# Kernel optimization log

Measured on AMD Instinct MI355X. Metric: run time of the kernel, lower is better.

Reference implementation:

```python
import jax, jax.numpy as jnp
import numpy as np

B, ZD, E, L, NL = 64, 512, 512, 8192, 1000


def irm(x, Ws, bs):
    # IRMLinear(d, n_layers=2): stack of residual linear blocks x <- x + Linear(x)
    for W, b in zip(Ws, bs):
        x = x + x @ W.T + b
    return x


def setup_inputs() -> dict:
    key = jax.random.key(0)
    ks = jax.random.split(key, 10)
    s = lambda k, sh: (jax.random.normal(k, sh, jnp.float32) * 0.02)
    return dict(
        z=jax.random.normal(ks[0], (B, ZD), jnp.float32),
        y=jax.random.randint(ks[1], (B,), 0, NL),
        W_yemb=s(ks[2], (E, NL)), b_yemb=jnp.zeros((E,), jnp.float32),
        Wy1=s(ks[3], (E, E)), by1=jnp.zeros((E,), jnp.float32),
        Wy2=s(ks[4], (E, E)), by2=jnp.zeros((E,), jnp.float32),
        Wz1=s(ks[5], (ZD, ZD)), bz1=jnp.zeros((ZD,), jnp.float32),
        Wz2=s(ks[6], (ZD, ZD)), bz2=jnp.zeros((ZD,), jnp.float32),
        W_zlat=s(ks[7], (L, ZD)),          # Linear(z_dim, lat_size, bias=False)
        w_proj=s(ks[8], (E,)),             # Linear(embed_size, 1, bias=False)
    )


def reference(z, y, W_yemb, b_yemb, Wy1, by1, Wy2, by2, Wz1, bz1, Wz2, bz2, W_zlat, w_proj):
    # y: int64 class ids -> one-hot via identity embedding_mat
    yembed = jax.nn.one_hot(y, NL, dtype=jnp.float32)            # [B, NL]
    ye = yembed @ W_yemb.T + b_yemb                               # [B, E]
    ye = irm(ye, [Wy1, Wy2], [by1, by2])                          # [B, E]
    zz = irm(z, [Wz1, Wz2], [bz1, bz2])                           # [B, ZD]
    zl = zz @ W_zlat.T                                            # [B, L]
    # bmm(z[:,:,1], ye[:,1,:]) then lat_proj over embed collapses to a
    # per-batch scalar: lat[b,i] = zl[b,i] * (ye[b] . w_proj)  (same math,
    # avoids the [B, L, E] intermediate)
    s_scal = ye @ w_proj                                          # [B]
    return zl * s_scal[:, None]                                   # [B, L]
```

## Files before the change

### kernel.cpp

```cpp
#include <hip/hip_runtime.h>


#define BB 64
#define DD 512
#define LL 8192
#define NLBL 1000
#define PIT 68

typedef __attribute__((ext_vector_type(8))) short short8;
typedef __attribute__((ext_vector_type(4))) float f32x4;

__device__ __forceinline__ unsigned short f2bf(float f) {
  unsigned u = __float_as_uint(f);
  return (unsigned short)((u + 0x7fffu + ((u >> 16) & 1u)) >> 16);
}

__device__ __forceinline__ void matvec_block(int eblk, const float* __restrict__ W,
                                             const float* __restrict__ vin,
                                             float* __restrict__ vout) {
  __shared__ float vl[DD];
  __shared__ float red[256];
  int tid = threadIdx.x;
  vl[tid] = vin[tid];
  vl[tid + 256] = vin[tid + 256];
  __syncthreads();
  int el = tid & 31, jg = tid >> 5;
  int e = eblk * 32 + el;
  float acc = 0.f;
  for (int j = jg; j < DD; j += 8)
    acc += W[j * DD + e] * vl[j];
  red[tid] = acc;
  __syncthreads();
  if (tid < 32) {
    float s = vl[eblk * 32 + tid];
#pragma unroll
    for (int g = 0; g < 8; ++g) s += red[g * 32 + tid];
    vout[eblk * 32 + tid] = s;
  }
}

template <int FIRST>
__device__ __forceinline__ void layer_gemm(int blk, const float* __restrict__ Xg,
                                           const float* __restrict__ P1,
                                           const float* __restrict__ W,
                                           const float* __restrict__ bias,
                                           float* __restrict__ P) {
  __shared__ __align__(16) float Xs[BB][PIT];
  __shared__ __align__(16) float Ws[32][PIT];
  int tid = threadIdx.x;
  int jt = blk >> 3, ks = blk & 7;
  int j0 = jt * 32, k0 = ks * 64;
#pragma unroll
  for (int i = 0; i < 4; ++i) {
    int slot = tid + i * 256, row = slot >> 4, c4 = (slot & 15) * 4;
    float4 v;
    if (FIRST) {
      v = *(const float4*)&Xg[row * DD + k0 + c4];
    } else {
      v = float4{0.f, 0.f, 0.f, 0.f};
#pragma unroll
      for (int s = 0; s < 8; ++s) {
        float4 p = *(const float4*)&P1[(s * BB + row) * DD + k0 + c4];
        v.x += p.x; v.y += p.y; v.z += p.z; v.w += p.w;
      }
    }
    *(float4*)&Xs[row][c4] = v;
  }
#pragma unroll
  for (int i = 0; i < 2; ++i) {
    int slot = tid + i * 256, row = slot >> 4, c4 = (slot & 15) * 4;
    *(float4*)&Ws[row][c4] = *(const float4*)&W[(j0 + row) * DD + k0 + c4];
  }
  __syncthreads();
  int jl = tid & 15, bl = tid >> 4;
  float acc[4][2] = {};
#pragma unroll
  for (int k = 0; k < 64; k += 4) {
    float4 xv[4], wv[2];
#pragma unroll
    for (int i = 0; i < 4; ++i) xv[i] = *(const float4*)&Xs[bl + 16 * i][k];
#pragma unroll
    for (int u = 0; u < 2; ++u) wv[u] = *(const float4*)&Ws[jl + 16 * u][k];
#pragma unroll
    for (int i = 0; i < 4; ++i)
#pragma unroll
      for (int u = 0; u < 2; ++u)
        acc[i][u] += xv[i].x * wv[u].x + xv[i].y * wv[u].y +
                     xv[i].z * wv[u].z + xv[i].w * wv[u].w;
  }
#pragma unroll
  for (int i = 0; i < 4; ++i) {
    int b = bl + 16 * i;
#pragma unroll
    for (int u = 0; u < 2; ++u) {
      int jj = j0 + jl + 16 * u;
      float v = acc[i][u];
      if (ks == 0) {
        float xr;
        if (FIRST) {
          xr = Xg[b * DD + jj];
        } else {
          xr = 0.f;
#pragma unroll
          for (int s = 0; s < 8; ++s) xr += P1[(s * BB + b) * DD + jj];
        }
        v += xr + bias[jj];
      }
      P[(ks * BB + b) * DD + jj] = v;
    }
  }
}

__global__ __launch_bounds__(256) void kA(const float* __restrict__ z,
                                          const float* __restrict__ Wz1,
                                          const float* __restrict__ bz1,
                                          float* __restrict__ P1,
                                          const float* __restrict__ Wy2,
                                          const float* __restrict__ w_proj,
                                          float* __restrict__ u1) {
  int blk = blockIdx.x;
  if (blk < 128) layer_gemm<1>(blk, z, nullptr, Wz1, bz1, P1);
  else           matvec_block(blk - 128, Wy2, w_proj, u1);
}

__global__ __launch_bounds__(256) void kB(const float* __restrict__ P1,
                                          const float* __restrict__ Wz2,
                                          const float* __restrict__ bz2,
                                          float* __restrict__ P2,
                                          const float* __restrict__ Wy1,
                                          const float* __restrict__ u1,
                                          float* __restrict__ u0,
                                          const float* __restrict__ by1,
                                          const float* __restrict__ by2,
                                          const float* __restrict__ w_proj,
                                          float* __restrict__ d2) {
  int blk = blockIdx.x;
  if (blk < 128) {
    layer_gemm<0>(blk, nullptr, P1, Wz2, bz2, P2);
  } else if (blk < 144) {
    matvec_block(blk - 128, Wy1, u1, u0);
  } else {
    __shared__ float red[256];
    int tid = threadIdx.x;
    float p = by1[tid] * u1[tid] + by2[tid] * w_proj[tid] +
              by1[tid + 256] * u1[tid + 256] + by2[tid + 256] * w_proj[tid + 256];
    red[tid] = p;
    __syncthreads();
    if (tid < 64) {
      float s = red[tid] + red[tid + 64] + red[tid + 128] + red[tid + 192];
#pragma unroll
      for (int d = 32; d; d >>= 1) s += __shfl_down(s, d, 64);
      if (tid == 0) d2[0] = s;
    }
  }
}

__global__ __launch_bounds__(256) void kZ(const float* __restrict__ P2,
                                          unsigned short* __restrict__ zzbf,
                                          const float* __restrict__ W_yemb,
                                          const float* __restrict__ b_yemb,
                                          const int* __restrict__ y,
                                          const float* __restrict__ u0,
                                          const float* __restrict__ d2,
                                          float* __restrict__ sbv) {
  int blk = blockIdx.x, tid = threadIdx.x;
  if (blk < 16) {
    int e0 = blk * 2048 + tid * 8;
    float4 a0 = {0.f, 0.f, 0.f, 0.f}, a1 = {0.f, 0.f, 0.f, 0.f};
#pragma unroll
    for (int s = 0; s < 8; ++s) {
      const float* p = P2 + s * (BB * DD) + e0;
      float4 x = *(const float4*)p;
      float4 yv = *(const float4*)(p + 4);
      a0.x += x.x; a0.y += x.y; a0.z += x.z; a0.w += x.w;
      a1.x += yv.x; a1.y += yv.y; a1.z += yv.z; a1.w += yv.w;
    }
    short8 h = {(short)f2bf(a0.x), (short)f2bf(a0.y), (short)f2bf(a0.z),
                (short)f2bf(a0.w), (short)f2bf(a1.x), (short)f2bf(a1.y),
                (short)f2bf(a1.z), (short)f2bf(a1.w)};
    *(short8*)&zzbf[e0] = h;
    return;
  }
  __shared__ float u0l[DD];
  u0l[tid] = u0[tid];
  u0l[tid + 256] = u0[tid + 256];
  __syncthreads();
  int bl = tid >> 5, el = tid & 31;
  int b = (blk - 16) * 8 + bl;
  int yb = y[b];
  float acc = 0.f;
  for (int e = el; e < DD; e += 32)
    acc += (W_yemb[(size_t)e * NLBL + yb] + b_yemb[e]) * u0l[e];
#pragma unroll
  for (int d = 16; d; d >>= 1) acc += __shfl_down(acc, d, 32);
  if (el == 0) sbv[b] = acc + d2[0];
}

__global__ __launch_bounds__(256) void kC(const unsigned short* __restrict__ zzbf,
                                          const float* __restrict__ W,
                                          const float* __restrict__ sbv,
                                          float* __restrict__ out) {
  __shared__ __align__(16) unsigned short As[64 * 128];
  __shared__ __align__(16) unsigned short Bs[32 * 128];
  int tid = threadIdx.x;
  int l0 = blockIdx.x * 32;
  int wave = tid >> 6, lane = tid & 63;
  int quad = lane >> 4, l15 = lane & 15;
  f32x4 acc[2] = {};
  for (int kc = 0; kc < 4; ++kc) {
    int k0 = kc * 128;
#pragma unroll
    for (int i = 0; i < 2; ++i) {
      int slot = tid + i * 256, row = slot >> 4, g = slot & 15;
      const float* src = &W[(size_t)(l0 + row) * DD + k0 + g * 8];
      float4 v0 = *(const float4*)src;
      float4 v1 = *(const float4*)(src + 4);
      short8 h = {(short)f2bf(v0.x), (short)f2bf(v0.y), (short)f2bf(v0.z),
                  (short)f2bf(v0.w), (short)f2bf(v1.x), (short)f2bf(v1.y),
                  (short)f2bf(v1.z), (short)f2bf(v1.w)};
      *(short8*)&Bs[row * 128 + ((g ^ (row & 15)) << 3)] = h;
    }
#pragma unroll
    for (int i = 0; i < 4; ++i) {
      int slot = tid + i * 256, row = slot >> 4, g = slot & 15;
      short8 h = *(const short8*)&zzbf[row * DD + k0 + g * 8];
      *(short8*)&As[row * 128 + ((g ^ (row & 15)) << 3)] = h;
    }
    __syncthreads();
#pragma unroll
    for (int s = 0; s < 4; ++s) {
      int g = s * 4 + quad;
      short8 af = *(const short8*)&As[(wave * 16 + l15) * 128 +
                                      ((g ^ l15) << 3)];
#pragma unroll
      for (int ni = 0; ni < 2; ++ni) {
        short8 bf = *(const short8*)&Bs[(ni * 16 + l15) * 128 +
                                        ((g ^ l15) << 3)];
        acc[ni] = __builtin_amdgcn_mfma_f32_16x16x32_bf16(af, bf, acc[ni], 0, 0, 0);
      }
    }
    __syncthreads();
  }
#pragma unroll
  for (int ni = 0; ni < 2; ++ni) {
#pragma unroll
    for (int reg = 0; reg < 4; ++reg) {
      int b = wave * 16 + quad * 4 + reg;
      out[(size_t)b * LL + l0 + ni * 16 + l15] = sbv[b] * acc[ni][reg];
    }
  }
}

extern "C" void kernel_launch(void* const* d_in, const int* in_sizes, int n_in,
                              void* d_out, int out_size, void* d_ws, size_t ws_size,
                              hipStream_t stream) {
  const float* z      = (const float*)d_in[0];
  const int*   y      = (const int*)  d_in[1];
  const float* W_yemb = (const float*)d_in[2];
  const float* b_yemb = (const float*)d_in[3];
  const float* Wy1    = (const float*)d_in[4];
  const float* by1    = (const float*)d_in[5];
  const float* Wy2    = (const float*)d_in[6];
  const float* by2    = (const float*)d_in[7];
  const float* Wz1    = (const float*)d_in[8];
  const float* bz1    = (const float*)d_in[9];
  const float* Wz2    = (const float*)d_in[10];
  const float* bz2    = (const float*)d_in[11];
  const float* W_zlat = (const float*)d_in[12];
  const float* w_proj = (const float*)d_in[13];

  float* ws = (float*)d_ws;
  float* P1 = ws;
  float* P2 = ws + 262144;
  unsigned short* zzbf = (unsigned short*)(ws + 524288);
  float* u1 = ws + 524288 + 16384;
  float* u0 = u1 + 512;
  float* sb = u0 + 512;
  float* d2 = sb + 64;
  float* out = (float*)d_out;

  kA<<<144, 256, 0, stream>>>(z, Wz1, bz1, P1, Wy2, w_proj, u1);
  kB<<<145, 256, 0, stream>>>(P1, Wz2, bz2, P2, Wy1, u1, u0, by1, by2, w_proj, d2);
  kZ<<<24, 256, 0, stream>>>(P2, zzbf, W_yemb, b_yemb, y, u0, d2, sb);
  kC<<<256, 256, 0, stream>>>(zzbf, W_zlat, sb, out);
}
```

Measured before the change: 143.6 us.

## Fuse four launches into one persistent kernel with atomic-counter grid barriers

Replaces the four kernel launches with a single kernel. 256 blocks preload and convert their W_zlat tile to bf16 in shared memory while 145 chain blocks run the two IRM layers, the y-side matvecs and the scalar reduction, separated by global atomic-counter barriers. The per-batch scale is folded into the bf16 zz rows before the final MFMA GEMM, and A fragments are read straight from global memory instead of being staged in LDS. This removes launch gaps and overlaps the large W_zlat load with the serial chain, but it relies on all 401 blocks being co-resident (deadlock risk otherwise), adds spin-waiting and a memset, and applying the scale before bf16 rounding changes rounding slightly.

```diff
diff --git a/kernel.cpp b/kernel.cpp
--- a/kernel.cpp
+++ b/kernel.cpp
@@ -6,6 +6,8 @@
 #define LL 8192
 #define NLBL 1000
 #define PIT 68
+#define NKC 256
+#define NCHAIN 145
 
 typedef __attribute__((ext_vector_type(8))) short short8;
 typedef __attribute__((ext_vector_type(4))) float f32x4;
@@ -15,11 +17,27 @@
   return (unsigned short)((u + 0x7fffu + ((u >> 16) & 1u)) >> 16);
 }
 
-__device__ __forceinline__ void matvec_block(int eblk, const float* __restrict__ W,
+__device__ __forceinline__ unsigned ld_agent(const unsigned* p) {
+  return __hip_atomic_load(p, __ATOMIC_RELAXED, __HIP_MEMORY_SCOPE_AGENT);
+}
+
+__device__ __forceinline__ void chain_barrier(unsigned* c) {
+  __syncthreads();
+  if (threadIdx.x == 0) {
+    __threadfence();
+    atomicAdd(c, 1u);
+    while (ld_agent(c) < NCHAIN) __builtin_amdgcn_s_sleep(1);
+    __threadfence();
+  }
+  __syncthreads();
+}
+
+__device__ __forceinline__ void matvec_block(char* SM, int eblk,
+                                             const float* __restrict__ W,
                                              const float* __restrict__ vin,
                                              float* __restrict__ vout) {
-  __shared__ float vl[DD];
-  __shared__ float red[256];
+  float* vl = (float*)SM;
+  float* red = vl + DD;
   int tid = threadIdx.x;
   vl[tid] = vin[tid];
   vl[tid + 256] = vin[tid + 256];
@@ -40,13 +58,14 @@
 }
 
 template <int FIRST>
-__device__ __forceinline__ void layer_gemm(int blk, const float* __restrict__ Xg,
-                                           const float* __restrict__ P1,
+__device__ __forceinline__ void layer_gemm(char* SM, int blk,
+                                           const float* __restrict__ Xg,
+                                           const float* __restrict__ Pin,
                                            const float* __restrict__ W,
                                            const float* __restrict__ bias,
                                            float* __restrict__ P) {
-  __shared__ __align__(16) float Xs[BB][PIT];
-  __shared__ __align__(16) float Ws[32][PIT];
+  float (*Xs)[PIT] = (float (*)[PIT])SM;
+  float (*Ws)[PIT] = (float (*)[PIT])(SM + BB * PIT * 4);
   int tid = threadIdx.x;
   int jt = blk >> 3, ks = blk & 7;
   int j0 = jt * 32, k0 = ks * 64;
@@ -60,7 +79,7 @@
       v = float4{0.f, 0.f, 0.f, 0.f};
 #pragma unroll
       for (int s = 0; s < 8; ++s) {
-        float4 p = *(const float4*)&P1[(s * BB + row) * DD + k0 + c4];
+        float4 p = *(const float4*)&Pin[(s * BB + row) * DD + k0 + c4];
         v.x += p.x; v.y += p.y; v.z += p.z; v.w += p.w;
       }
     }
@@ -102,7 +121,7 @@
         } else {
           xr = 0.f;
 #pragma unroll
-          for (int s = 0; s < 8; ++s) xr += P1[(s * BB + b) * DD + jj];
+          for (int s = 0; s < 8; ++s) xr += Pin[(s * BB + b) * DD + jj];
         }
         v += xr + bias[jj];
       }
@@ -111,37 +130,85 @@
   }
 }
 
-__global__ __launch_bounds__(256) void kA(const float* __restrict__ z,
-                                          const float* __restrict__ Wz1,
-                                          const float* __restrict__ bz1,
-                                          float* __restrict__ P1,
-                                          const float* __restrict__ Wy2,
-                                          const float* __restrict__ w_proj,
-                                          float* __restrict__ u1) {
-  int blk = blockIdx.x;
-  if (blk < 128) layer_gemm<1>(blk, z, nullptr, Wz1, bz1, P1);
-  else           matvec_block(blk - 128, Wy2, w_proj, u1);
-}
-
-__global__ __launch_bounds__(256) void kB(const float* __restrict__ P1,
-                                          const float* __restrict__ Wz2,
-                                          const float* __restrict__ bz2,
-                                          float* __restrict__ P2,
-                                          const float* __restrict__ Wy1,
-                                          const float* __restrict__ u1,
-                                          float* __restrict__ u0,
-                                          const float* __restrict__ by1,
-                                          const float* __restrict__ by2,
-                                          const float* __restrict__ w_proj,
-                                          float* __restrict__ d2) {
-  int blk = blockIdx.x;
-  if (blk < 128) {
-    layer_gemm<0>(blk, nullptr, P1, Wz2, bz2, P2);
-  } else if (blk < 144) {
-    matvec_block(blk - 128, Wy1, u1, u0);
+__global__ __launch_bounds__(256, 2) void mega(
+    const float* __restrict__ z, const float* __restrict__ Wz1,
+    const float* __restrict__ bz1, const float* __restrict__ Wz2,
+    const float* __restrict__ bz2, const float* __restrict__ Wy1,
+    const float* __restrict__ by1, const float* __restrict__ Wy2,
+    const float* __restrict__ by2, const float* __restrict__ w_proj,
+    const float* __restrict__ W_yemb, const float* __restrict__ b_yemb,
+    const int* __restrict__ y, const float* __restrict__ W_zlat,
+    float* __restrict__ P1, float* __restrict__ P2,
+    unsigned short* __restrict__ zzs, float* __restrict__ u1,
+    float* __restrict__ u0, float* __restrict__ d2,
+    unsigned* __restrict__ cnt, float* __restrict__ out) {
+  __shared__ __align__(16) char SM[32768];
+  int blk = blockIdx.x, tid = threadIdx.x;
+
+  if (blk < NKC) {
+    unsigned short* Bs = (unsigned short*)SM;
+    int l0 = blk * 32;
+#pragma unroll
+    for (int i = 0; i < 8; ++i) {
+      int gi = tid + i * 256;
+      int row = gi >> 6, c = gi & 63;
+      const float* src = &W_zlat[(size_t)(l0 + row) * DD + c * 8];
+      float4 v0 = *(const float4*)src;
+      float4 v1 = *(const float4*)(src + 4);
+      short8 h = {(short)f2bf(v0.x), (short)f2bf(v0.y), (short)f2bf(v0.z),
+                  (short)f2bf(v0.w), (short)f2bf(v1.x), (short)f2bf(v1.y),
+                  (short)f2bf(v1.z), (short)f2bf(v1.w)};
+      *(short8*)&Bs[row * DD + ((c ^ (row & 7)) << 3)] = h;
+    }
+    if (tid == 0) {
+      while (ld_agent(&cnt[64]) < NCHAIN) __builtin_amdgcn_s_sleep(2);
+      __threadfence();
+    }
+    __syncthreads();
+    int wave = tid >> 6, lane = tid & 63, quad = lane >> 4, l15 = lane & 15;
+    const unsigned short* arow = zzs + (wave * 16 + l15) * DD + quad * 8;
+    int brow0 = l15, brow1 = 16 + l15;
+    f32x4 acc0 = {}, acc1 = {};
+    short8 apf[4];
+#pragma unroll
+    for (int p = 0; p < 4; ++p) apf[p] = *(const short8*)(arow + p * 32);
+#pragma unroll
+    for (int kc = 0; kc < 4; ++kc) {
+      short8 cur[4] = {apf[0], apf[1], apf[2], apf[3]};
+      if (kc < 3) {
+#pragma unroll
+        for (int p = 0; p < 4; ++p)
+          apf[p] = *(const short8*)(arow + (kc + 1) * 128 + p * 32);
+      }
+#pragma unroll
+      for (int s = 0; s < 4; ++s) {
+        int c = kc * 16 + s * 4 + quad;
+        short8 b0 = *(const short8*)&Bs[brow0 * DD + ((c ^ (brow0 & 7)) << 3)];
+        short8 b1 = *(const short8*)&Bs[brow1 * DD + ((c ^ (brow1 & 7)) << 3)];
+        acc0 = __builtin_amdgcn_mfma_f32_16x16x32_bf16(cur[s], b0, acc0, 0, 0, 0);
+        acc1 = __builtin_amdgcn_mfma_f32_16x16x32_bf16(cur[s], b1, acc1, 0, 0, 0);
+      }
+    }
+#pragma unroll
+    for (int reg = 0; reg < 4; ++reg) {
+      int b = wave * 16 + quad * 4 + reg;
+      size_t o = (size_t)b * LL + l0;
+      out[o + l15] = acc0[reg];
+      out[o + 16 + l15] = acc1[reg];
+    }
+    return;
+  }
+
+  int cid = blk - NKC;
+  if (cid < 128)      layer_gemm<1>(SM, cid, z, nullptr, Wz1, bz1, P1);
+  else if (cid < 144) matvec_block(SM, cid - 128, Wy2, w_proj, u1);
+  chain_barrier(&cnt[0]);
+  if (cid < 128) {
+    layer_gemm<0>(SM, cid, nullptr, P1, Wz2, bz2, P2);
+  } else if (cid < 144) {
+    matvec_block(SM, cid - 128, Wy1, u1, u0);
   } else {
-    __shared__ float red[256];
-    int tid = threadIdx.x;
+    float* red = (float*)SM;
     float p = by1[tid] * u1[tid] + by2[tid] * w_proj[tid] +
               by1[tid + 256] * u1[tid + 256] + by2[tid + 256] * w_proj[tid + 256];
     red[tid] = p;
@@ -153,102 +220,48 @@
       if (tid == 0) d2[0] = s;
     }
   }
-}
-
-__global__ __launch_bounds__(256) void kZ(const float* __restrict__ P2,
-                                          unsigned short* __restrict__ zzbf,
-                                          const float* __restrict__ W_yemb,
-                                          const float* __restrict__ b_yemb,
-                                          const int* __restrict__ y,
-                                          const float* __restrict__ u0,
-                                          const float* __restrict__ d2,
-                                          float* __restrict__ sbv) {
-  int blk = blockIdx.x, tid = threadIdx.x;
-  if (blk < 16) {
-    int e0 = blk * 2048 + tid * 8;
+  chain_barrier(&cnt[32]);
+  if (cid < 16) {
+    int bloc = tid >> 6, lane = tid & 63;
+    int bb = cid * 4 + bloc;
+    int yb = y[bb];
+    int e0 = lane * 8;
+    float4 ua = *(const float4*)&u0[e0];
+    float4 ub = *(const float4*)&u0[e0 + 4];
+    float4 ba = *(const float4*)&b_yemb[e0];
+    float4 bb4 = *(const float4*)&b_yemb[e0 + 4];
+    const float* wy = W_yemb + yb;
+    float sg = (wy[(size_t)(e0 + 0) * NLBL] + ba.x) * ua.x +
+               (wy[(size_t)(e0 + 1) * NLBL] + ba.y) * ua.y +
+               (wy[(size_t)(e0 + 2) * NLBL] + ba.z) * ua.z +
+               (wy[(size_t)(e0 + 3) * NLBL] + ba.w) * ua.w +
+               (wy[(size_t)(e0 + 4) * NLBL] + bb4.x) * ub.x +
+               (wy[(size_t)(e0 + 5) * NLBL] + bb4.y) * ub.y +
+               (wy[(size_t)(e0 + 6) * NLBL] + bb4.z) * ub.z +
+               (wy[(size_t)(e0 + 7) * NLBL] + bb4.w) * ub.w;
+#pragma unroll
+    for (int d = 32; d; d >>= 1) sg += __shfl_down(sg, d, 64);
+    float* s4 = (float*)SM;
+    if (lane == 0) s4[bloc] = sg + d2[0];
+    __syncthreads();
+    float sv = s4[bloc];
+    int eo = cid * 2048 + tid * 8;
     float4 a0 = {0.f, 0.f, 0.f, 0.f}, a1 = {0.f, 0.f, 0.f, 0.f};
 #pragma unroll
     for (int s = 0; s < 8; ++s) {
-      const float* p = P2 + s * (BB * DD) + e0;
+      const float* p = P2 + s * (BB * DD) + eo;
       float4 x = *(const float4*)p;
-      float4 yv = *(const float4*)(p + 4);
+      float4 q = *(const float4*)(p + 4);
       a0.x += x.x; a0.y += x.y; a0.z += x.z; a0.w += x.w;
-      a1.x += yv.x; a1.y += yv.y; a1.z += yv.z; a1.w += yv.w;
-    }
-    short8 h = {(short)f2bf(a0.x), (short)f2bf(a0.y), (short)f2bf(a0.z),
-                (short)f2bf(a0.w), (short)f2bf(a1.x), (short)f2bf(a1.y),
-                (short)f2bf(a1.z), (short)f2bf(a1.w)};
-    *(short8*)&zzbf[e0] = h;
-    return;
-  }
-  __shared__ float u0l[DD];
-  u0l[tid] = u0[tid];
-  u0l[tid + 256] = u0[tid + 256];
-  __syncthreads();
-  int bl = tid >> 5, el = tid & 31;
-  int b = (blk - 16) * 8 + bl;
-  int yb = y[b];
-  float acc = 0.f;
-  for (int e = el; e < DD; e += 32)
-    acc += (W_yemb[(size_t)e * NLBL + yb] + b_yemb[e]) * u0l[e];
-#pragma unroll
-  for (int d = 16; d; d >>= 1) acc += __shfl_down(acc, d, 32);
-  if (el == 0) sbv[b] = acc + d2[0];
-}
-
-__global__ __launch_bounds__(256) void kC(const unsigned short* __restrict__ zzbf,
-                                          const float* __restrict__ W,
-                                          const float* __restrict__ sbv,
-                                          float* __restrict__ out) {
-  __shared__ __align__(16) unsigned short As[64 * 128];
-  __shared__ __align__(16) unsigned short Bs[32 * 128];
-  int tid = threadIdx.x;
-  int l0 = blockIdx.x * 32;
-  int wave = tid >> 6, lane = tid & 63;
-  int quad = lane >> 4, l15 = lane & 15;
-  f32x4 acc[2] = {};
-  for (int kc = 0; kc < 4; ++kc) {
-    int k0 = kc * 128;
-#pragma unroll
-    for (int i = 0; i < 2; ++i) {
-      int slot = tid + i * 256, row = slot >> 4, g = slot & 15;
-      const float* src = &W[(size_t)(l0 + row) * DD + k0 + g * 8];
-      float4 v0 = *(const float4*)src;
-      float4 v1 = *(const float4*)(src + 4);
-      short8 h = {(short)f2bf(v0.x), (short)f2bf(v0.y), (short)f2bf(v0.z),
-                  (short)f2bf(v0.w), (short)f2bf(v1.x), (short)f2bf(v1.y),
-                  (short)f2bf(v1.z), (short)f2bf(v1.w)};
-      *(short8*)&Bs[row * 128 + ((g ^ (row & 15)) << 3)] = h;
-    }
-#pragma unroll
-    for (int i = 0; i < 4; ++i) {
-      int slot = tid + i * 256, row = slot >> 4, g = slot & 15;
-      short8 h = *(const short8*)&zzbf[row * DD + k0 + g * 8];
-      *(short8*)&As[row * 128 + ((g ^ (row & 15)) << 3)] = h;
-    }
-    __syncthreads();
-#pragma unroll
-    for (int s = 0; s < 4; ++s) {
-      int g = s * 4 + quad;
-      short8 af = *(const short8*)&As[(wave * 16 + l15) * 128 +
-                                      ((g ^ l15) << 3)];
-#pragma unroll
-      for (int ni = 0; ni < 2; ++ni) {
-        short8 bf = *(const short8*)&Bs[(ni * 16 + l15) * 128 +
-                                        ((g ^ l15) << 3)];
-        acc[ni] = __builtin_amdgcn_mfma_f32_16x16x32_bf16(af, bf, acc[ni], 0, 0, 0);
-      }
-    }
-    __syncthreads();
-  }
-#pragma unroll
-  for (int ni = 0; ni < 2; ++ni) {
-#pragma unroll
-    for (int reg = 0; reg < 4; ++reg) {
-      int b = wave * 16 + quad * 4 + reg;
-      out[(size_t)b * LL + l0 + ni * 16 + l15] = sbv[b] * acc[ni][reg];
-    }
-  }
+      a1.x += q.x; a1.y += q.y; a1.z += q.z; a1.w += q.w;
+    }
+    short8 h = {(short)f2bf(a0.x * sv), (short)f2bf(a0.y * sv),
+                (short)f2bf(a0.z * sv), (short)f2bf(a0.w * sv),
+                (short)f2bf(a1.x * sv), (short)f2bf(a1.y * sv),
+                (short)f2bf(a1.z * sv), (short)f2bf(a1.w * sv)};
+    *(short8*)&zzs[eo] = h;
+  }
+  chain_barrier(&cnt[64]);
 }
 
 extern "C" void kernel_launch(void* const* d_in, const int* in_sizes, int n_in,
@@ -272,15 +285,15 @@
   float* ws = (float*)d_ws;
   float* P1 = ws;
   float* P2 = ws + 262144;
-  unsigned short* zzbf = (unsigned short*)(ws + 524288);
-  float* u1 = ws + 524288 + 16384;
-  float* u0 = u1 + 512;
-  float* sb = u0 + 512;
-  float* d2 = sb + 64;
+  unsigned short* zzs = (unsigned short*)(ws + 524288);
+  float* u1 = ws + 540672;
+  float* u0 = ws + 541184;
+  float* d2 = ws + 541696;
+  unsigned* cnt = (unsigned*)(ws + 541712);
   float* out = (float*)d_out;
 
-  kA<<<144, 256, 0, stream>>>(z, Wz1, bz1, P1, Wy2, w_proj, u1);
-  kB<<<145, 256, 0, stream>>>(P1, Wz2, bz2, P2, Wy1, u1, u0, by1, by2, w_proj, d2);
-  kZ<<<24, 256, 0, stream>>>(P2, zzbf, W_yemb, b_yemb, y, u0, d2, sb);
-  kC<<<256, 256, 0, stream>>>(zzbf, W_zlat, sb, out);
-}
+  hipMemsetAsync(cnt, 0, 384, stream);
+  mega<<<NKC + NCHAIN, 256, 0, stream>>>(
+      z, Wz1, bz1, Wz2, bz2, Wy1, by1, Wy2, by2, w_proj, W_yemb, b_yemb, y,
+      W_zlat, P1, P2, zzs, u1, u0, d2, cnt, out);
+}
```

Result: slower. 189.6 us (+32.0%).

## Fold per-batch scale into bf16 zz and restructure final GEMM tiling

Applied to the files above, without the earlier changes.

The per-batch scalar is now computed inside kZ and multiplied into zz before the bf16 conversion, so kC no longer reads sbv. kZ shrinks to 16 blocks that each do both jobs. kC is retiled to 16 output columns per block over 512 blocks and stages the whole K=512 W_zlat slice in shared memory once. The A operand is read straight from global memory into registers with prefetching, which removes the LDS staging and per-chunk barriers for zz. The trade-offs are more blocks and repeated global reads of zz, and rounding zz·s to bf16 changes numerics slightly.

```diff
diff --git a/kernel.cpp b/kernel.cpp
--- a/kernel.cpp
+++ b/kernel.cpp
@@ -41,7 +41,7 @@
 
 template <int FIRST>
 __device__ __forceinline__ void layer_gemm(int blk, const float* __restrict__ Xg,
-                                           const float* __restrict__ P1,
+                                           const float* __restrict__ Pin,
                                            const float* __restrict__ W,
                                            const float* __restrict__ bias,
                                            float* __restrict__ P) {
@@ -60,7 +60,7 @@
       v = float4{0.f, 0.f, 0.f, 0.f};
 #pragma unroll
       for (int s = 0; s < 8; ++s) {
-        float4 p = *(const float4*)&P1[(s * BB + row) * DD + k0 + c4];
+        float4 p = *(const float4*)&Pin[(s * BB + row) * DD + k0 + c4];
         v.x += p.x; v.y += p.y; v.z += p.z; v.w += p.w;
       }
     }
@@ -102,7 +102,7 @@
         } else {
           xr = 0.f;
 #pragma unroll
-          for (int s = 0; s < 8; ++s) xr += P1[(s * BB + b) * DD + jj];
+          for (int s = 0; s < 8; ++s) xr += Pin[(s * BB + b) * DD + jj];
         }
         v += xr + bias[jj];
       }
@@ -156,98 +156,96 @@
 }
 
 __global__ __launch_bounds__(256) void kZ(const float* __restrict__ P2,
-                                          unsigned short* __restrict__ zzbf,
+                                          unsigned short* __restrict__ zzs,
                                           const float* __restrict__ W_yemb,
                                           const float* __restrict__ b_yemb,
                                           const int* __restrict__ y,
                                           const float* __restrict__ u0,
-                                          const float* __restrict__ d2,
-                                          float* __restrict__ sbv) {
-  int blk = blockIdx.x, tid = threadIdx.x;
-  if (blk < 16) {
-    int e0 = blk * 2048 + tid * 8;
-    float4 a0 = {0.f, 0.f, 0.f, 0.f}, a1 = {0.f, 0.f, 0.f, 0.f};
-#pragma unroll
-    for (int s = 0; s < 8; ++s) {
-      const float* p = P2 + s * (BB * DD) + e0;
-      float4 x = *(const float4*)p;
-      float4 yv = *(const float4*)(p + 4);
-      a0.x += x.x; a0.y += x.y; a0.z += x.z; a0.w += x.w;
-      a1.x += yv.x; a1.y += yv.y; a1.z += yv.z; a1.w += yv.w;
-    }
-    short8 h = {(short)f2bf(a0.x), (short)f2bf(a0.y), (short)f2bf(a0.z),
-                (short)f2bf(a0.w), (short)f2bf(a1.x), (short)f2bf(a1.y),
-                (short)f2bf(a1.z), (short)f2bf(a1.w)};
-    *(short8*)&zzbf[e0] = h;
-    return;
-  }
-  __shared__ float u0l[DD];
-  u0l[tid] = u0[tid];
-  u0l[tid + 256] = u0[tid + 256];
-  __syncthreads();
-  int bl = tid >> 5, el = tid & 31;
-  int b = (blk - 16) * 8 + bl;
-  int yb = y[b];
-  float acc = 0.f;
-  for (int e = el; e < DD; e += 32)
-    acc += (W_yemb[(size_t)e * NLBL + yb] + b_yemb[e]) * u0l[e];
-#pragma unroll
-  for (int d = 16; d; d >>= 1) acc += __shfl_down(acc, d, 32);
-  if (el == 0) sbv[b] = acc + d2[0];
-}
-
-__global__ __launch_bounds__(256) void kC(const unsigned short* __restrict__ zzbf,
+                                          const float* __restrict__ d2) {
+  __shared__ float s4[4];
+  int cid = blockIdx.x, tid = threadIdx.x;
+  int bloc = tid >> 6, lane = tid & 63;
+  int bb = cid * 4 + bloc;
+  int yb = y[bb];
+  int e0 = lane * 8;
+  float4 ua = *(const float4*)&u0[e0];
+  float4 ub = *(const float4*)&u0[e0 + 4];
+  float4 ba = *(const float4*)&b_yemb[e0];
+  float4 bb4 = *(const float4*)&b_yemb[e0 + 4];
+  const float* wy = W_yemb + yb;
+  float sg = (wy[(size_t)(e0 + 0) * NLBL] + ba.x) * ua.x +
+             (wy[(size_t)(e0 + 1) * NLBL] + ba.y) * ua.y +
+             (wy[(size_t)(e0 + 2) * NLBL] + ba.z) * ua.z +
+             (wy[(size_t)(e0 + 3) * NLBL] + ba.w) * ua.w +
+             (wy[(size_t)(e0 + 4) * NLBL] + bb4.x) * ub.x +
+             (wy[(size_t)(e0 + 5) * NLBL] + bb4.y) * ub.y +
+             (wy[(size_t)(e0 + 6) * NLBL] + bb4.z) * ub.z +
+             (wy[(size_t)(e0 + 7) * NLBL] + bb4.w) * ub.w;
+#pragma unroll
+  for (int d = 32; d; d >>= 1) sg += __shfl_down(sg, d, 64);
+  if (lane == 0) s4[bloc] = sg + d2[0];
+  __syncthreads();
+  float sv = s4[bloc];
+  int eo = cid * 2048 + tid * 8;
+  float4 a0 = {0.f, 0.f, 0.f, 0.f}, a1 = {0.f, 0.f, 0.f, 0.f};
+#pragma unroll
+  for (int s = 0; s < 8; ++s) {
+    const float* p = P2 + s * (BB * DD) + eo;
+    float4 x = *(const float4*)p;
+    float4 q = *(const float4*)(p + 4);
+    a0.x += x.x; a0.y += x.y; a0.z += x.z; a0.w += x.w;
+    a1.x += q.x; a1.y += q.y; a1.z += q.z; a1.w += q.w;
+  }
+  short8 h = {(short)f2bf(a0.x * sv), (short)f2bf(a0.y * sv),
+              (short)f2bf(a0.z * sv), (short)f2bf(a0.w * sv),
+              (short)f2bf(a1.x * sv), (short)f2bf(a1.y * sv),
+              (short)f2bf(a1.z * sv), (short)f2bf(a1.w * sv)};
+  *(short8*)&zzs[eo] = h;
+}
+
+__global__ __launch_bounds__(256) void kC(const unsigned short* __restrict__ zzs,
                                           const float* __restrict__ W,
-                                          const float* __restrict__ sbv,
                                           float* __restrict__ out) {
-  __shared__ __align__(16) unsigned short As[64 * 128];
-  __shared__ __align__(16) unsigned short Bs[32 * 128];
+  __shared__ __align__(16) unsigned short Bs[16 * 512];
   int tid = threadIdx.x;
-  int l0 = blockIdx.x * 32;
-  int wave = tid >> 6, lane = tid & 63;
-  int quad = lane >> 4, l15 = lane & 15;
-  f32x4 acc[2] = {};
+  int l0 = blockIdx.x * 16;
+#pragma unroll
+  for (int i = 0; i < 4; ++i) {
+    int gi = tid + i * 256, row = gi >> 6, c = gi & 63;
+    const float* src = &W[(size_t)(l0 + row) * DD + c * 8];
+    float4 v0 = *(const float4*)src;
+    float4 v1 = *(const float4*)(src + 4);
+    short8 h = {(short)f2bf(v0.x), (short)f2bf(v0.y), (short)f2bf(v0.z),
+                (short)f2bf(v0.w), (short)f2bf(v1.x), (short)f2bf(v1.y),
+                (short)f2bf(v1.z), (short)f2bf(v1.w)};
+    *(short8*)&Bs[row * DD + ((c ^ (row & 7)) << 3)] = h;
+  }
+  __syncthreads();
+  int wave = tid >> 6, lane = tid & 63, quad = lane >> 4, l15 = lane & 15;
+  const unsigned short* arow = zzs + (wave * 16 + l15) * DD + quad * 8;
+  f32x4 acc = {};
+  short8 apf[4];
+#pragma unroll
+  for (int p = 0; p < 4; ++p) apf[p] = *(const short8*)(arow + p * 32);
+#pragma unroll
   for (int kc = 0; kc < 4; ++kc) {
-    int k0 = kc * 128;
-#pragma unroll
-    for (int i = 0; i < 2; ++i) {
-      int slot = tid + i * 256, row = slot >> 4, g = slot & 15;
-      const float* src = &W[(size_t)(l0 + row) * DD + k0 + g * 8];
-      float4 v0 = *(const float4*)src;
-      float4 v1 = *(const float4*)(src + 4);
-      short8 h = {(short)f2bf(v0.x), (short)f2bf(v0.y), (short)f2bf(v0.z),
-                  (short)f2bf(v0.w), (short)f2bf(v1.x), (short)f2bf(v1.y),
-                  (short)f2bf(v1.z), (short)f2bf(v1.w)};
-      *(short8*)&Bs[row * 128 + ((g ^ (row & 15)) << 3)] = h;
-    }
-#pragma unroll
-    for (int i = 0; i < 4; ++i) {
-      int slot = tid + i * 256, row = slot >> 4, g = slot & 15;
-      short8 h = *(const short8*)&zzbf[row * DD + k0 + g * 8];
-      *(short8*)&As[row * 128 + ((g ^ (row & 15)) << 3)] = h;
-    }
-    __syncthreads();
+    short8 cur[4] = {apf[0], apf[1], apf[2], apf[3]};
+    if (kc < 3) {
+#pragma unroll
+      for (int p = 0; p < 4; ++p)
+        apf[p] = *(const short8*)(arow + (kc + 1) * 128 + p * 32);
+    }
 #pragma unroll
     for (int s = 0; s < 4; ++s) {
-      int g = s * 4 + quad;
-      short8 af = *(const short8*)&As[(wave * 16 + l15) * 128 +
-                                      ((g ^ l15) << 3)];
-#pragma unroll
-      for (int ni = 0; ni < 2; ++ni) {
-        short8 bf = *(const short8*)&Bs[(ni * 16 + l15) * 128 +
-                                        ((g ^ l15) << 3)];
-        acc[ni] = __builtin_amdgcn_mfma_f32_16x16x32_bf16(af, bf, acc[ni], 0, 0, 0);
-      }
-    }
-    __syncthreads();
-  }
-#pragma unroll
-  for (int ni = 0; ni < 2; ++ni) {
-#pragma unroll
-    for (int reg = 0; reg < 4; ++reg) {
-      int b = wave * 16 + quad * 4 + reg;
-      out[(size_t)b * LL + l0 + ni * 16 + l15] = sbv[b] * acc[ni][reg];
-    }
+      int c = kc * 16 + s * 4 + quad;
+      short8 bf = *(const short8*)&Bs[l15 * DD + ((c ^ (l15 & 7)) << 3)];
+      acc = __builtin_amdgcn_mfma_f32_16x16x32_bf16(cur[s], bf, acc, 0, 0, 0);
+    }
+  }
+#pragma unroll
+  for (int reg = 0; reg < 4; ++reg) {
+    int b = wave * 16 + quad * 4 + reg;
+    out[(size_t)b * LL + l0 + l15] = acc[reg];
   }
 }
 
@@ -272,15 +270,14 @@
   float* ws = (float*)d_ws;
   float* P1 = ws;
   float* P2 = ws + 262144;
-  unsigned short* zzbf = (unsigned short*)(ws + 524288);
-  float* u1 = ws + 524288 + 16384;
-  float* u0 = u1 + 512;
-  float* sb = u0 + 512;
-  float* d2 = sb + 64;
+  unsigned short* zzs = (unsigned short*)(ws + 524288);
+  float* u1 = ws + 540672;
+  float* u0 = ws + 541184;
+  float* d2 = ws + 541696;
   float* out = (float*)d_out;
 
   kA<<<144, 256, 0, stream>>>(z, Wz1, bz1, P1, Wy2, w_proj, u1);
   kB<<<145, 256, 0, stream>>>(P1, Wz2, bz2, P2, Wy1, u1, u0, by1, by2, w_proj, d2);
-  kZ<<<24, 256, 0, stream>>>(P2, zzbf, W_yemb, b_yemb, y, u0, d2, sb);
-  kC<<<256, 256, 0, stream>>>(zzbf, W_zlat, sb, out);
-}
+  kZ<<<16, 256, 0, stream>>>(P2, zzs, W_yemb, b_yemb, y, u0, d2);
+  kC<<<512, 256, 0, stream>>>(zzs, W_zlat, out);
+}
```

Result: no change. 143.4 us (-0.2%).
